# Kernel optimization log

Hardware: AMD Instinct MI355X
Metric: run time of the kernel (lower is better)

## Reference

```python
import jax, jax.numpy as jnp
import numpy as np

GROUPS = 8
EPS = 1e-5


def setup_inputs() -> dict:
    key = jax.random.key(0)
    ks = jax.random.split(key, 7)
    B, C, H, W = 16, 512, 32, 32
    x = jax.random.normal(ks[0], (B, C, H, W), dtype=jnp.float32)
    norm_w = jnp.ones((C,), jnp.float32)
    norm_b = jnp.zeros((C,), jnp.float32)
    qkv_w = jax.random.normal(ks[1], (3 * C, C), dtype=jnp.float32) * (1.0 / np.sqrt(C))
    qkv_b = jnp.zeros((3 * C,), jnp.float32)
    proj_w = jax.random.normal(ks[2], (C, C), dtype=jnp.float32) * (1.0 / np.sqrt(C))
    proj_b = jnp.zeros((C,), jnp.float32)
    num_heads = 8
    return {"x": x, "norm_w": norm_w, "norm_b": norm_b, "qkv_w": qkv_w,
            "qkv_b": qkv_b, "proj_w": proj_w, "proj_b": proj_b,
            "num_heads": num_heads}


def reference(x, norm_w, norm_b, qkv_w, qkv_b, proj_w, proj_b, num_heads):
    b, c, h, w = x.shape
    n = h * w
    x_in = x
    # GroupNorm(8, c): normalize over (channels-in-group, spatial)
    xg = x.reshape(b, GROUPS, c // GROUPS, n)
    mean = jnp.mean(xg, axis=(2, 3), keepdims=True)
    var = jnp.var(xg, axis=(2, 3), keepdims=True)
    xn = (xg - mean) * jax.lax.rsqrt(var + EPS)
    xn = xn.reshape(b, c, n) * norm_w[None, :, None] + norm_b[None, :, None]
    # 1x1 Conv1d == per-position matmul
    qkv = jnp.einsum('oc,bcn->bon', qkv_w, xn) + qkv_b[None, :, None]
    q, k, v = jnp.split(qkv, 3, axis=1)
    d = c // num_heads
    q = q.reshape(b, num_heads, d, n)
    k = k.reshape(b, num_heads, d, n)
    v = v.reshape(b, num_heads, d, n)
    scale = 1.0 / np.sqrt(d).astype(np.float32)
    # note: scale applied to BOTH q and k (as in the torch source)
    attn = jnp.einsum('bhdn,bhdm->bhnm', q * scale, k * scale)
    attn = jax.nn.softmax(attn, axis=-1)
    out = jnp.einsum('bhnm,bhdm->bhdn', attn, v).reshape(b, c, n)
    out = jnp.einsum('oc,bcn->bon', proj_w, out) + proj_b[None, :, None]
    return out.reshape(b, c, h, w) + x_in
```

## Files before the change

### kernel.cpp

```cpp
#include <hip/hip_runtime.h>

#define NB 16
#define NC 512
#define NSP 1024
#define OQKV 1536
#define EPSV 1e-5f

typedef unsigned short u16;
typedef unsigned int u32;
typedef __attribute__((ext_vector_type(8))) short short8;
typedef __attribute__((ext_vector_type(4))) float f32x4;
typedef __attribute__((ext_vector_type(16))) float f32x16;

__device__ __forceinline__ float us2f(u16 u) {
  return __uint_as_float(((u32)u) << 16);
}
__device__ __forceinline__ u16 f2us(float f) {
  u32 x = __float_as_uint(f);
  return (u16)((x + 0x7fffu + ((x >> 16) & 1u)) >> 16);
}
#if __has_builtin(__builtin_amdgcn_cvt_pk_bf16_f32)
typedef __attribute__((ext_vector_type(2))) __bf16 bf16x2_t;
__device__ __forceinline__ u32 pack2(float a, float b) {
  bf16x2_t r = __builtin_amdgcn_cvt_pk_bf16_f32(a, b);
  return *reinterpret_cast<u32*>(&r);
}
#else
__device__ __forceinline__ u32 pack2(float a, float b) {
  return (u32)f2us(a) | ((u32)f2us(b) << 16);
}
#endif
__device__ __forceinline__ float fexp2(float x) {
#if __has_builtin(__builtin_amdgcn_exp2f)
  return __builtin_amdgcn_exp2f(x);
#else
  return __expf(x * 0.6931471805599453f);
#endif
}
__device__ __forceinline__ float ld1(const void* p, size_t i, bool f32) {
  return f32 ? ((const float*)p)[i] : us2f(((const u16*)p)[i]);
}
__device__ __forceinline__ bool detect_f32(const void* x0) {
  const u32* xw = (const u32*)x0;
  u32 w = xw[threadIdx.x & 63];
  u32 e = ((w & 0xffffu) >> 7) & 0xffu;
  bool sane = (e >= 0x60u && e <= 0x9fu);
  return __popcll(__ballot(sane)) < 32;
}

typedef const __attribute__((address_space(1))) unsigned int* gas_t;
typedef __attribute__((address_space(3))) unsigned int* las_t;
__device__ __forceinline__ void gload16(const void* g, void* l) {
  __builtin_amdgcn_global_load_lds((gas_t)g, (las_t)l, 16, 0, 0);
}

__global__ __launch_bounds__(256) void gn_partial(
    const void* __restrict__ x, float2* __restrict__ part) {
  bool f32 = detect_f32(x);
  int idx = blockIdx.x;
  size_t base = (size_t)idx * 32768;
  float s1 = 0.f, s2 = 0.f;
  for (int i = threadIdx.x; i < 4096; i += 256) {
    float f[8];
    if (f32) {
      float4 a = *((const float4*)x + (base >> 2) + i * 2);
      float4 b = *((const float4*)x + (base >> 2) + i * 2 + 1);
      f[0]=a.x; f[1]=a.y; f[2]=a.z; f[3]=a.w; f[4]=b.x; f[5]=b.y; f[6]=b.z; f[7]=b.w;
    } else {
      uint4 p = *((const uint4*)x + (base >> 3) + i);
      f[0]=us2f((u16)(p.x&0xffffu)); f[1]=us2f((u16)(p.x>>16));
      f[2]=us2f((u16)(p.y&0xffffu)); f[3]=us2f((u16)(p.y>>16));
      f[4]=us2f((u16)(p.z&0xffffu)); f[5]=us2f((u16)(p.z>>16));
      f[6]=us2f((u16)(p.w&0xffffu)); f[7]=us2f((u16)(p.w>>16));
    }
#pragma unroll
    for (int m = 0; m < 8; m++) { s1 += f[m]; s2 += f[m] * f[m]; }
  }
  __shared__ float r1[256], r2[256];
  r1[threadIdx.x] = s1; r2[threadIdx.x] = s2;
  __syncthreads();
  for (int s = 128; s > 0; s >>= 1) {
    if ((int)threadIdx.x < s) {
      r1[threadIdx.x] += r1[threadIdx.x + s];
      r2[threadIdx.x] += r2[threadIdx.x + s];
    }
    __syncthreads();
  }
  if (threadIdx.x == 0) part[idx] = make_float2(r1[0], r2[0]);
}

__global__ __launch_bounds__(256) void prep_all(
    const void* __restrict__ x, const float2* __restrict__ part,
    const void* __restrict__ gamma, const void* __restrict__ beta,
    const void* __restrict__ qkvw, const void* __restrict__ projw,
    u16* __restrict__ wq, u16* __restrict__ wp, u16* __restrict__ xnt) {
  bool f32 = detect_f32(x);
  int p = blockIdx.x;
  int t = threadIdx.x;
  if (p < 512) {
    const void* src = (p < 384) ? qkvw : projw;
    u16* dst = (p < 384) ? wq : wp;
    size_t e = ((size_t)(p < 384 ? p : p - 384) * 256 + t) * 8;
    uint4 v;
    if (f32) {
      float4 a = *(const float4*)((const float*)src + e);
      float4 b = *(const float4*)((const float*)src + e + 4);
      v.x = pack2(a.x, a.y); v.y = pack2(a.z, a.w);
      v.z = pack2(b.x, b.y); v.w = pack2(b.z, b.w);
    } else {
      v = *(const uint4*)((const u16*)src + e);
    }
    *(uint4*)(dst + e) = v;
    return;
  }
  int q = p - 512;
  int b = q >> 7;
  int c0 = ((q >> 4) & 7) << 6;
  int n0 = (q & 15) << 6;
  __shared__ __align__(16) u16 T[64 * 64];
  int cc = t >> 4;
  int nn = (t & 15) << 2;
  float2 pa = part[((b << 3) + (c0 >> 6)) * 2];
  float2 pb = part[((b << 3) + (c0 >> 6)) * 2 + 1];
  float mean = (pa.x + pb.x) * (1.f / 65536.f);
  float var = (pa.y + pb.y) * (1.f / 65536.f) - mean * mean;
  float inv = rsqrtf(var + EPSV);
#pragma unroll
  for (int rep = 0; rep < 4; rep++) {
    int cl = cc + (rep << 4);
    int c = c0 + cl;
    float g = ld1(gamma, c, f32), be = ld1(beta, c, f32);
    float wsc = g * inv, bsc = be - mean * wsc;
    size_t xb = ((size_t)b * NC + c) * NSP + n0 + nn;
    float f[4];
    if (f32) {
      float4 v = *(const float4*)((const float*)x + xb);
      f[0]=v.x; f[1]=v.y; f[2]=v.z; f[3]=v.w;
    } else {
      uint2 v = *(const uint2*)((const u16*)x + xb);
      f[0]=us2f((u16)(v.x&0xffffu)); f[1]=us2f((u16)(v.x>>16));
      f[2]=us2f((u16)(v.y&0xffffu)); f[3]=us2f((u16)(v.y>>16));
    }
#pragma unroll
    for (int j = 0; j < 4; j++) {
      int n = nn + j;
      T[(n << 6) + (((cl & ~7) ^ ((n & 7) << 3)) | (cl & 7))] =
          f2us(fmaf(f[j], wsc, bsc));
    }
  }
  __syncthreads();
#pragma unroll
  for (int i = 0; i < 2; i++) {
    int slot = (i << 8) + t;
    int nl = slot >> 3;
    int cs = (slot & 7) << 3;
    uint4 v = *(const uint4*)&T[(nl << 6) + (cs ^ ((nl & 7) << 3))];
    *(uint4*)&xnt[((size_t)b * NSP + n0 + nl) * NC + c0 + cs] = v;
  }
}

template <bool OUTRAW, bool RES>
__global__ __launch_bounds__(256) void mfma_gemm(
    const u16* __restrict__ W, const u16* __restrict__ Xt,
    const void* __restrict__ xdet, const void* __restrict__ bias,
    const void* __restrict__ res, void* __restrict__ out, int O) {
  bool f32 = detect_f32(xdet);
  bool of = OUTRAW && f32;
  int gy = O >> 7;
  int bpb = gy << 3;
  int p = blockIdx.x + (blockIdx.y << 3) + blockIdx.z * bpb;
  int k = p >> 3;
  int b = ((p & 7) << 1) + (k >= bpb ? 1 : 0);
  int r = k - (k >= bpb ? bpb : 0);
  int orow = (r >> 3) << 7;
  int ncol = (r & 7) << 7;
  int t = threadIdx.x;
  int lane = t & 63, w = t >> 6;
  int wo = (w >> 1) << 6, wn = (w & 1) << 6;
  int l15 = lane & 15, quad = lane >> 4;

  __shared__ __align__(16) u16 Alds[128 * 64];
  __shared__ __align__(16) u16 Blds[128 * 64];

  f32x4 acc[4][4];
#pragma unroll
  for (int i = 0; i < 4; i++)
#pragma unroll
    for (int j = 0; j < 4; j++) acc[i][j] = (f32x4){0.f, 0.f, 0.f, 0.f};

  int srow = t >> 3;
  int seg = (t & 7) ^ (srow & 7);
  const u16* wpA = W + (size_t)(orow + srow) * NC + (seg << 3);
  const u16* xpB = Xt + ((size_t)b * NSP + ncol + srow) * NC + (seg << 3);

  for (int k0 = 0; k0 < NC; k0 += 64) {
    __syncthreads();
#pragma unroll
    for (int i = 0; i < 4; i++) {
      gload16(wpA + k0 + (size_t)i * (32 * NC), &Alds[(i << 11) + (w << 9)]);
      gload16(xpB + k0 + (size_t)i * (32 * NC), &Blds[(i << 11) + (w << 9)]);
    }
    __syncthreads();
#pragma unroll
    for (int kk = 0; kk < 2; kk++) {
      short8 af[4], bf[4];
#pragma unroll
      for (int ot = 0; ot < 4; ot++) {
        int rr = wo + ot * 16 + l15;
        af[ot] = *(const short8*)&Alds[(rr << 6) + ((((kk << 2) + quad) ^ (rr & 7)) << 3)];
      }
#pragma unroll
      for (int nt = 0; nt < 4; nt++) {
        int rr = wn + nt * 16 + l15;
        bf[nt] = *(const short8*)&Blds[(rr << 6) + ((((kk << 2) + quad) ^ (rr & 7)) << 3)];
      }
#pragma unroll
      for (int ot = 0; ot < 4; ot++)
#pragma unroll
        for (int nt = 0; nt < 4; nt++)
          acc[ot][nt] = __builtin_amdgcn_mfma_f32_16x16x32_bf16(
              af[ot], bf[nt], acc[ot][nt], 0, 0, 0);
    }
  }
#pragma unroll
  for (int ot = 0; ot < 4; ot++) {
#pragma unroll
    for (int rr = 0; rr < 4; rr++) {
      int o = orow + wo + ot * 16 + (quad << 2) + rr;
      float bs = ld1(bias, o, f32);
      size_t rowb = ((size_t)b * O + o) * NSP + ncol + wn + l15;
#pragma unroll
      for (int nt = 0; nt < 4; nt++) {
        size_t idx = rowb + nt * 16;
        float v = acc[ot][nt][rr] + bs;
        if (RES) v += ld1(res, idx, f32);
        if (of) ((float*)out)[idx] = v;
        else ((u16*)out)[idx] = f2us(v);
      }
    }
  }
}

__global__ __launch_bounds__(512, 4) void attn_kernel(
    const u16* __restrict__ qkv, u16* __restrict__ OT) {
  int d = blockIdx.x;
  int blk = ((((d & 7) << 4) | (d >> 5)) << 2) | ((d >> 3) & 3);
  int b = blk >> 5;
  int hh = (blk >> 2) & 7;
  int q0 = (blk & 3) << 8;
  int t = threadIdx.x;
  int lane = t & 63, w = t >> 6;
  int l31 = lane & 31, hl = lane >> 5;

  __shared__ __align__(16) u16 Klds[2][64 * 72];
  __shared__ __align__(16) u16 Vlds[2][64 * 72];

  size_t hb = (size_t)b * OQKV + hh * 64;
  int qrow = q0 + (w << 5) + l31;

  const float QSC = 1.442695041f / 64.f;
  short8 qf[4];
#pragma unroll
  for (int ks = 0; ks < 4; ks++)
#pragma unroll
    for (int j = 0; j < 8; j++) {
      int dd = ks * 16 + (hl << 3) + j;
      qf[ks][j] = (short)f2us(us2f(qkv[(hb + dd) * NSP + qrow]) * QSC);
    }

  short8 onesf;
#pragma unroll
  for (int j = 0; j < 8; j++) onesf[j] = (short)0x3F80;

  f32x16 oacc[2], lsacc;
#pragma unroll
  for (int dt = 0; dt < 2; dt++)
#pragma unroll
    for (int e = 0; e < 16; e++) oacc[dt][e] = 0.f;
#pragma unroll
  for (int e = 0; e < 16; e++) lsacc[e] = 0.f;

  bool isK = (t < 256);
  int ts = t & 255;
  int m0k = (ts & 15) << 2;
  int d0k = (ts >> 4) << 2;
  int sdv = ts >> 2;
  int sm0 = (ts & 3) << 4;
  const u16* kbase = qkv + (hb + 512) * NSP;
  const u16* vbase = qkv + (hb + 1024 + sdv) * NSP;

  uint2 kr[4];
  uint4 vr0, vr1;
  auto preload = [&](int mc) {
    if (isK) {
#pragma unroll
      for (int i = 0; i < 4; i++)
        kr[i] = *(const uint2*)(kbase + (size_t)(d0k + i) * NSP + mc + m0k);
    } else {
      vr0 = *(const uint4*)(vbase + mc + sm0);
      vr1 = *(const uint4*)(vbase + mc + sm0 + 8);
    }
  };

  preload(0);
  int cur = 0;
  for (int mc = 0; mc < NSP; mc += 64) {
    if (isK) {
#pragma unroll
      for (int j = 0; j < 4; j++) {
        u32 s0 = (j & 2) ? kr[0].y : kr[0].x;
        u32 s1 = (j & 2) ? kr[1].y : kr[1].x;
        u32 s2 = (j & 2) ? kr[2].y : kr[2].x;
        u32 s3 = (j & 2) ? kr[3].y : kr[3].x;
        int sh = (j & 1) << 4;
        uint2 wv;
        wv.x = ((s0 >> sh) & 0xffffu) | (((s1 >> sh) & 0xffffu) << 16);
        wv.y = ((s2 >> sh) & 0xffffu) | (((s3 >> sh) & 0xffffu) << 16);
        *(uint2*)&Klds[cur][(m0k + j) * 72 + d0k] = wv;
      }
    } else {
      *(uint4*)&Vlds[cur][sdv * 72 + sm0] = vr0;
      *(uint4*)&Vlds[cur][sdv * 72 + sm0 + 8] = vr1;
    }
    __syncthreads();
    if (mc + 64 < NSP) preload(mc + 64);
#pragma unroll
    for (int mt = 0; mt < 2; mt++) {
      f32x16 s;
#pragma unroll
      for (int e = 0; e < 16; e++) s[e] = 0.f;
#pragma unroll
      for (int ks = 0; ks < 4; ks++) {
        short8 kf = *(const short8*)&Klds[cur][((mt << 5) + l31) * 72 + (ks << 4) + (hl << 3)];
        s = __builtin_amdgcn_mfma_f32_32x32x16_bf16(kf, qf[ks], s, 0, 0, 0);
      }
      u32 pk[8];
#pragma unroll
      for (int i = 0; i < 8; i++) {
        float e0 = fexp2(s[2 * i]), e1 = fexp2(s[2 * i + 1]);
        pk[i] = pack2(e0, e1);
      }
      short8 pf[2];
#pragma unroll
      for (int ks2 = 0; ks2 < 2; ks2++) {
        u32 a0 = pk[4 * ks2 + 2], b0 = pk[4 * ks2 + 0];
        u32 a1 = pk[4 * ks2 + 3], b1 = pk[4 * ks2 + 1];
        asm volatile("v_permlane32_swap_b32 %0, %1" : "+v"(a0), "+v"(b0));
        asm volatile("v_permlane32_swap_b32 %0, %1" : "+v"(a1), "+v"(b1));
        uint4 wv;
        wv.x = b0;
        wv.y = b1;
        wv.z = a0;
        wv.w = a1;
        pf[ks2] = *reinterpret_cast<short8*>(&wv);
      }
#pragma unroll
      for (int ks2 = 0; ks2 < 2; ks2++) {
        lsacc = __builtin_amdgcn_mfma_f32_32x32x16_bf16(onesf, pf[ks2], lsacc, 0, 0, 0);
#pragma unroll
        for (int dt = 0; dt < 2; dt++) {
          short8 vf = *(const short8*)&Vlds[cur][((dt << 5) + l31) * 72 + (mt << 5) + (ks2 << 4) + (hl << 3)];
          oacc[dt] = __builtin_amdgcn_mfma_f32_32x32x16_bf16(vf, pf[ks2], oacc[dt], 0, 0, 0);
        }
      }
    }
    cur ^= 1;
  }
  float invL = 1.0f / lsacc[0];
  u16* op = OT + ((size_t)b * NSP + qrow) * NC + (hh << 6);
#pragma unroll
  for (int dt = 0; dt < 2; dt++)
#pragma unroll
    for (int g = 0; g < 4; g++) {
      uint2 pw;
      pw.x = pack2(oacc[dt][4 * g + 0] * invL, oacc[dt][4 * g + 1] * invL);
      pw.y = pack2(oacc[dt][4 * g + 2] * invL, oacc[dt][4 * g + 3] * invL);
      *(uint2*)&op[(dt << 5) + (g << 3) + (hl << 2)] = pw;
    }
}

extern "C" void kernel_launch(void* const* d_in, const int* in_sizes, int n_in,
                              void* d_out, int out_size, void* d_ws, size_t ws_size,
                              hipStream_t stream) {
  const void* x      = d_in[0];
  const void* norm_w = d_in[1];
  const void* norm_b = d_in[2];
  const void* qkv_w  = d_in[3];
  const void* qkv_b  = d_in[4];
  const void* proj_w = d_in[5];
  const void* proj_b = d_in[6];

  char* ws = (char*)d_ws;
  float2* part  = (float2*)ws;
  u16* qkv = (u16*)(ws + 4096);
  u16* xnt = (u16*)(ws + 4096 + 50331648);
  u16* wq  = (u16*)(ws + 4096 + 50331648 + 16777216);
  u16* wp  = wq + OQKV * NC;

  gn_partial<<<256, 256, 0, stream>>>(x, part);
  prep_all<<<2560, 256, 0, stream>>>(x, part, norm_w, norm_b,
                                     qkv_w, proj_w, wq, wp, xnt);
  mfma_gemm<false, false><<<dim3(8, 12, NB), 256, 0, stream>>>(
      wq, xnt, x, qkv_b, nullptr, qkv, OQKV);
  attn_kernel<<<512, 512, 0, stream>>>(qkv, xnt );
  mfma_gemm<true, true><<<dim3(8, 4, NB), 256, 0, stream>>>(
      wp, xnt, x, proj_b, x, d_out, NC);
}
```

Before: 225.3 us.

## Deepen K/V prefetch to two register stages in attention loop

Replaces the single register prefetch of the next K/V tile with two register sets (A/B) and a loop unrolled by two. Each global load is now issued a full tile earlier, giving more latency hiding across the compute phase. V loads change from two 16-byte loads to four 8-byte loads so both stages share one layout. This costs extra registers, which may lower occupancy, and it keeps only a single barrier per stage.

Result: slower. 232.4 us (+3.1%).

```diff
diff --git a/kernel.cpp b/kernel.cpp
--- a/kernel.cpp
+++ b/kernel.cpp
@@ -289,29 +289,27 @@
   const u16* kbase = qkv + (hb + 512) * NSP;
   const u16* vbase = qkv + (hb + 1024 + sdv) * NSP;
 
-  uint2 kr[4];
-  uint4 vr0, vr1;
-  auto preload = [&](int mc) {
+  uint2 sA[4], sB[4];
+  auto preloadA = [&](int mc) {
+#pragma unroll
+    for (int i = 0; i < 4; i++)
+      sA[i] = isK ? *(const uint2*)(kbase + (size_t)(d0k + i) * NSP + mc + m0k)
+                  : *(const uint2*)(vbase + mc + sm0 + (i << 2));
+  };
+  auto preloadB = [&](int mc) {
+#pragma unroll
+    for (int i = 0; i < 4; i++)
+      sB[i] = isK ? *(const uint2*)(kbase + (size_t)(d0k + i) * NSP + mc + m0k)
+                  : *(const uint2*)(vbase + mc + sm0 + (i << 2));
+  };
+  auto stage = [&](int cur, const uint2* s) {
     if (isK) {
 #pragma unroll
-      for (int i = 0; i < 4; i++)
-        kr[i] = *(const uint2*)(kbase + (size_t)(d0k + i) * NSP + mc + m0k);
-    } else {
-      vr0 = *(const uint4*)(vbase + mc + sm0);
-      vr1 = *(const uint4*)(vbase + mc + sm0 + 8);
-    }
-  };
-
-  preload(0);
-  int cur = 0;
-  for (int mc = 0; mc < NSP; mc += 64) {
-    if (isK) {
-#pragma unroll
       for (int j = 0; j < 4; j++) {
-        u32 s0 = (j & 2) ? kr[0].y : kr[0].x;
-        u32 s1 = (j & 2) ? kr[1].y : kr[1].x;
-        u32 s2 = (j & 2) ? kr[2].y : kr[2].x;
-        u32 s3 = (j & 2) ? kr[3].y : kr[3].x;
+        u32 s0 = (j & 2) ? s[0].y : s[0].x;
+        u32 s1 = (j & 2) ? s[1].y : s[1].x;
+        u32 s2 = (j & 2) ? s[2].y : s[2].x;
+        u32 s3 = (j & 2) ? s[3].y : s[3].x;
         int sh = (j & 1) << 4;
         uint2 wv;
         wv.x = ((s0 >> sh) & 0xffffu) | (((s1 >> sh) & 0xffffu) << 16);
@@ -319,11 +317,12 @@
         *(uint2*)&Klds[cur][(m0k + j) * 72 + d0k] = wv;
       }
     } else {
-      *(uint4*)&Vlds[cur][sdv * 72 + sm0] = vr0;
-      *(uint4*)&Vlds[cur][sdv * 72 + sm0 + 8] = vr1;
-    }
-    __syncthreads();
-    if (mc + 64 < NSP) preload(mc + 64);
+#pragma unroll
+      for (int i = 0; i < 4; i++)
+        *(uint2*)&Vlds[cur][sdv * 72 + sm0 + (i << 2)] = s[i];
+    }
+  };
+  auto compute = [&](int cur) {
 #pragma unroll
     for (int mt = 0; mt < 2; mt++) {
       f32x16 s;
@@ -364,7 +363,19 @@
         }
       }
     }
-    cur ^= 1;
+  };
+
+  preloadA(0);
+  preloadB(64);
+  for (int mc = 0; mc < NSP; mc += 128) {
+    stage(0, sA);
+    __syncthreads();
+    if (mc + 128 < NSP) preloadA(mc + 128);
+    compute(0);
+    stage(1, sB);
+    __syncthreads();
+    if (mc + 192 < NSP) preloadB(mc + 192);
+    compute(1);
   }
   float invL = 1.0f / lsacc[0];
   u16* op = OT + ((size_t)b * NSP + qrow) * NC + (hh << 6);
```
